# Kernel tuning notes

Measured on AMD Instinct MI355X. Metric: run time of the kernel, lower is better.

The kernel has to match this reference:

```python
import jax, jax.numpy as jnp
import numpy as np

N = 768        # nodes
F = 64         # invariant (0e) hidden channels
V = 16         # vector (1e) hidden channels
NB = 8         # bessel basis size
HR = 64        # radial MLP hidden
T = 2          # interactions
RO_S = 32      # invariant readout channels
RO_V = 16      # vector readout channels
RMAX = 10.0
AVG = float(N - 1)   # avg_num_neighbors (fully connected)
P = F + V + F + V + V  # tensor-product paths: s*Y0->0e, dot(v,Y1)->0e, s*Y1->1e, v*Y0->1e, cross(v,Y1)->1e


def _edges(n):
    # fully connected neighbor list (cut_off = 1e6, no pbc): all i != j
    s, r = np.meshgrid(np.arange(n), np.arange(n), indexing='ij')
    m = s != r
    return jnp.asarray(s[m]), jnp.asarray(r[m])


def _bessel(r):
    # bessel_basis(number=NB): sqrt(2/r_max) * sin(n*pi*r/r_max) / r
    n = jnp.arange(1, NB + 1, dtype=r.dtype)
    return jnp.sqrt(2.0 / RMAX) * jnp.sin(n * jnp.pi * r[:, None] / RMAX) / r[:, None]


def _envelope(r):
    # soft_envelope: 1.2 * sus(2*(1 - r/r_max)), sus(u) = exp(-1/u) for u>0 else 0
    u = 2.0 * (1.0 - r / RMAX)
    safe = jnp.where(u > 0, u, 1.0)
    return 1.2 * jnp.where(u > 0, jnp.exp(-1.0 / safe), 0.0)


def setup_inputs() -> dict:
    key = jax.random.key(0)
    ks = jax.random.split(key, 12)
    rn = lambda k, shp, fan: jax.random.normal(k, shp, jnp.float32) / np.sqrt(fan)
    return {
        'x': jax.random.normal(ks[0], (N, 3), jnp.float32),
        'embed': rn(ks[1], (1, F), 1),
        'w_node_s': rn(ks[2], (T, F, F), F),
        'w_node_v': rn(ks[3], (T, V, V), V),
        'w_rad1': rn(ks[4], (T, NB, HR), NB),
        'b_rad1': jnp.zeros((T, HR), jnp.float32),
        'w_rad2': rn(ks[5], (T, HR, P), HR),
        'w_mix_s': rn(ks[6], (T, F + V, F), F + V),
        'w_mix_v': rn(ks[7], (T, F + 2 * V, V), F + 2 * V),
        'w_gate': rn(ks[8], (T, F, V), F),
        'w_ro_s': rn(ks[9], (T, F, RO_S), F),
        'w_ro_v': rn(ks[10], (T, V, RO_V), V),
    }


def reference(x, embed, w_node_s, w_node_v, w_rad1, b_rad1, w_rad2,
              w_mix_s, w_mix_v, w_gate, w_ro_s, w_ro_v):
    n = x.shape[0]
    com = jnp.mean(x, axis=-2)                       # [3] centre of mass
    senders, receivers = _edges(n)
    vec = x[receivers] - x[senders]                  # [E,3] edge relative vectors
    r = jnp.linalg.norm(vec, axis=-1)                # [E]
    rhat = vec / r[:, None]                          # Y1 spherical harmonics (l=1)
    rb = _bessel(r)                                  # [E,NB]
    env = _envelope(r)                               # [E]

    h_s = jnp.broadcast_to(embed[0], (n, F))         # species embedding (all species 0)
    h_v = jnp.zeros((n, V, 3), x.dtype)
    out_s = jnp.zeros((n, RO_S), x.dtype)
    out_v = jnp.zeros((n, RO_V, 3), x.dtype)

    for t in range(T):
        # node-wise linear before gather
        hs = h_s @ w_node_s[t]                                    # [N,F]
        hv = jnp.einsum('nvc,vw->nwc', h_v, w_node_v[t])          # [N,V,3]
        es = hs[senders]                                          # [E,F]
        ev = hv[senders]                                          # [E,V,3]
        # per-edge tensor-product path weights from radial MLP, enveloped
        R = jax.nn.silu(rb @ w_rad1[t] + b_rad1[t]) @ w_rad2[t] * env[:, None]  # [E,P]
        r1, r2, r3, r4, r5 = (R[:, :F], R[:, F:F + V], R[:, F + V:2 * F + V],
                              R[:, 2 * F + V:2 * F + 2 * V], R[:, 2 * F + 2 * V:])
        # equivariant tensor products with Y0=1, Y1=rhat
        dot = jnp.einsum('evc,ec->ev', ev, rhat)                  # 1e x 1e -> 0e
        msg_s = jnp.concatenate([es * r1, dot * r2], axis=-1)     # [E,F+V]
        v1 = (es * r3)[:, :, None] * rhat[:, None, :]             # 0e x 1e -> 1e  [E,F,3]
        v2 = ev * r4[:, :, None]                                  # 1e x 0e -> 1e  [E,V,3]
        v3 = jnp.cross(ev, rhat[:, None, :]) * r5[:, :, None]     # 1e x 1e -> 1e  [E,V,3]
        msg_v = jnp.concatenate([v1, v2, v3], axis=1)             # [E,F+2V,3]
        # scatter-aggregate to receivers
        agg_s = jax.ops.segment_sum(msg_s, receivers, num_segments=n) / AVG
        agg_v = jax.ops.segment_sum(msg_v, receivers, num_segments=n) / AVG
        # mix + gated nonlinearity
        m_s = agg_s @ w_mix_s[t]                                  # [N,F]
        m_v = jnp.einsum('npc,pv->nvc', agg_v, w_mix_v[t])        # [N,V,3]
        h_s = jax.nn.silu(m_s)
        gate = jax.nn.sigmoid(m_s @ w_gate[t])                    # [N,V]
        h_v = gate[:, :, None] * m_v
        # readout (summed over interactions)
        out_s = out_s + h_s @ w_ro_s[t]
        out_v = out_v + jnp.einsum('nvc,vk->nkc', h_v, w_ro_v[t])

    return out_s, out_v + com
```

## Files before the change

### kernel.cpp

```cpp
#include <hip/hip_runtime.h>
#include <hip/hip_bf16.h>
#include <math.h>

#define Nn 768
#define Ff 64
#define Vv 16
#define NBb 8
#define HRr 64
#define Pp 176
#define TBL 1024
#define ROWC 176
#define RMAXF 10.0f
#define AVGF 767.0f
#define SCALE 102.4f

#define WS_COM   0
#define WS_ES0   16
#define WS_XP    128
#define WS_HSB   4096
#define WS_HVB   28672
#define WS_OS    53248
#define WS_OV    77824
#define WS_SLAB0 131072
#define WS_SLAB1 917504
#define WS_TBL   2097152

__device__ __forceinline__ unsigned short f2bf(float f) {
  unsigned b = __float_as_uint(f);
  return (unsigned short)((b + 0x7fffu + ((b >> 16) & 1u)) >> 16);
}
__device__ __forceinline__ float lp(unsigned u, float f) {
  float a = __uint_as_float(u << 16);
  float b = __uint_as_float(u & 0xffff0000u);
  return fmaf(f, b - a, a);
}
__device__ __forceinline__ float bl(unsigned u) { return __uint_as_float(u << 16); }
__device__ __forceinline__ float bh(unsigned u) { return __uint_as_float(u & 0xffff0000u); }

__global__ __launch_bounds__(256) void k_setup(const float* __restrict__ x,
                                               const float* __restrict__ embed,
                                               const float* __restrict__ wns,
                                               const float* __restrict__ w1,
                                               const float* __restrict__ b1,
                                               const float* __restrict__ w2,
                                               float* __restrict__ ws) {
  const int b = blockIdx.x, tid = threadIdx.x;
  if (b >= 256) {
    if (b == 256) {
      __shared__ float red[256][3];
      float a0 = 0, a1 = 0, a2 = 0;
      for (int n = tid; n < Nn; n += 256) {
        a0 += x[n * 3 + 0]; a1 += x[n * 3 + 1]; a2 += x[n * 3 + 2];
      }
      red[tid][0] = a0; red[tid][1] = a1; red[tid][2] = a2;
      __syncthreads();
      if (tid < 3) {
        float a = 0;
        for (int k = 0; k < 256; ++k) a += red[k][tid];
        ws[WS_COM + tid] = a * (1.0f / Nn);
      }
    } else if (b == 257) {
      for (int n = tid; n < Nn; n += 256) {
        ws[WS_XP + n * 4 + 0] = x[n * 3 + 0];
        ws[WS_XP + n * 4 + 1] = x[n * 3 + 1];
        ws[WS_XP + n * 4 + 2] = x[n * 3 + 2];
        ws[WS_XP + n * 4 + 3] = 0.0f;
      }
    } else {
      if (tid < 64) {
        float a = 0;
        for (int k = 0; k < 64; ++k) a = fmaf(embed[k], wns[k * 64 + tid], a);
        ws[WS_ES0 + tid] = a;
      }
    }
    return;
  }
  __shared__ float w2s[64][Pp];
  __shared__ float w1s[NBb][64];
  __shared__ float b1s[64];
  __shared__ float hid[9][65];
  const int t = b >> 7;
  const int r0 = (b & 127) * 8;
  const float* W2 = w2 + t * HRr * Pp;
  for (int k = tid; k < 64 * Pp; k += 256) w2s[k / Pp][k % Pp] = W2[k];
  for (int k = tid; k < NBb * 64; k += 256) w1s[k >> 6][k & 63] = w1[t * NBb * 64 + k];
  if (tid < 64) b1s[tid] = b1[t * 64 + tid];
  __syncthreads();
  {
    int rl4 = tid >> 6, h = tid & 63;
    const float c0 = 0.447213595f;
    const float pif = 3.14159265358979f;
    for (int pass = 0; pass < 3; ++pass) {
      int row_l = pass * 4 + rl4;
      if (row_l < 9) {
        int row = r0 + row_l;
        float r = row * (RMAXF / TBL);
        float acc = b1s[h];
        if (row == 0) {
          for (int n = 0; n < NBb; ++n) acc = fmaf(c0 * (n + 1) * (pif / RMAXF), w1s[n][h], acc);
        } else {
          float inv = 1.0f / r;
          for (int n = 0; n < NBb; ++n)
            acc = fmaf(c0 * sinf((n + 1) * pif * r / RMAXF) * inv, w1s[n][h], acc);
        }
        hid[row_l][h] = acc / (1.0f + expf(-acc));
      }
    }
  }
  __syncthreads();
  unsigned* T = (unsigned*)(ws + WS_TBL) + t * 1025 * ROWC;
  const int rl = tid & 7, colg = tid >> 3;
  const int rowa = r0 + rl;
  float ra = rowa * (RMAXF / TBL), rb = (rowa + 1) * (RMAXF / TBL);
  float ua = 2.0f * (1.0f - ra / RMAXF), ub = 2.0f * (1.0f - rb / RMAXF);
  float env_a = (ua > 0.0f) ? 1.2f * expf(-1.0f / ua) : 0.0f;
  float env_b = (ub > 0.0f) ? 1.2f * expf(-1.0f / ub) : 0.0f;
  float accA[6], accB[6];
  int pcol[6]; bool vc[6];
#pragma unroll
  for (int c = 0; c < 6; ++c) {
    int col = colg * 6 + c;
    bool valid = (col < 176);
    int p = 0;
    if (valid) {
      if (col < 64) p = col;
      else if (col < 128) p = 80 + (col - 64);
      else if (col < 144) p = 64 + (col - 128);
      else p = col;
    }
    pcol[c] = p; vc[c] = valid; accA[c] = 0.0f; accB[c] = 0.0f;
  }
  for (int h = 0; h < 64; ++h) {
    float ha = hid[rl][h], hb = hid[rl + 1][h];
#pragma unroll
    for (int c = 0; c < 6; ++c) {
      float w = w2s[h][pcol[c]];
      accA[c] = fmaf(ha, w, accA[c]);
      accB[c] = fmaf(hb, w, accB[c]);
    }
  }
#pragma unroll
  for (int c = 0; c < 6; ++c) {
    if (vc[c]) {
      int col = colg * 6 + c;
      float va = accA[c] * env_a;
      float vb = accB[c] * env_b;
      T[rowa * ROWC + col] = ((unsigned)f2bf(vb) << 16) | (unsigned)f2bf(va);
    }
  }
  if ((b & 127) == 127) {
    for (int k = tid; k < ROWC; k += 256) T[1024 * ROWC + k] = 0u;
  }
}

__global__ __launch_bounds__(256) void k_edge0(float* __restrict__ ws) {
  const int blk = blockIdx.x, i = blk >> 2, part = blk & 3;
  const int tid = threadIdx.x;
  const int w = tid >> 6, lane = tid & 63, sq = (lane >> 4) & 3, idx = lane & 15;
  __shared__ float4 GEO[192];
  __shared__ float wb[4][16][17];
  const float4* XP4 = (const float4*)(ws + WS_XP);
  const unsigned* T0 = (const unsigned*)(ws + WS_TBL);
  const float4 xi = XP4[i];
  if (tid < 192) {
    int j = part * 192 + tid;
    float4 xj = XP4[j];
    float dx = xi.x - xj.x, dy = xi.y - xj.y, dz = xi.z - xj.z;
    float r2 = dx * dx + dy * dy + dz * dz;
    float u, hx, hy, hz;
    if (j == i || r2 <= 0.0f) { u = 1024.0f; hx = hy = hz = 0.0f; }
    else {
      float rinv = rsqrtf(r2);
      hx = dx * rinv; hy = dy * rinv; hz = dz * rinv;
      u = fminf(r2 * rinv * SCALE, 1024.0f);
    }
    GEO[tid] = make_float4(hx, hy, hz, u);
  }
  __syncthreads();
  float s1[4] = {0, 0, 0, 0};
  float v1[4][3] = {};
  const int base = w * 48 + sq;
  float4 g = GEO[base];
  int i0 = (int)g.w;
  float fr = g.w - (float)i0;
  const uint4* rp = (const uint4*)(T0 + i0 * ROWC);
  uint4 t1 = rp[idx];
  uint4 t3 = rp[16 + idx];
  for (int q = 0; q < 12; ++q) {
    float4 gc = g; float frc = fr;
    uint4 t1c = t1, t3c = t3;
    if (q < 11) {
      g = GEO[base + (q + 1) * 4];
      i0 = (int)g.w;
      fr = g.w - (float)i0;
      const uint4* rpn = (const uint4*)(T0 + i0 * ROWC);
      t1 = rpn[idx];
      t3 = rpn[16 + idx];
    }
    s1[0] += lp(t1c.x, frc); s1[1] += lp(t1c.y, frc);
    s1[2] += lp(t1c.z, frc); s1[3] += lp(t1c.w, frc);
    float ax = lp(t3c.x, frc), ay = lp(t3c.y, frc), az = lp(t3c.z, frc), aw = lp(t3c.w, frc);
    v1[0][0] += ax * gc.x; v1[0][1] += ax * gc.y; v1[0][2] += ax * gc.z;
    v1[1][0] += ay * gc.x; v1[1][1] += ay * gc.y; v1[1][2] += ay * gc.z;
    v1[2][0] += az * gc.x; v1[2][1] += az * gc.y; v1[2][2] += az * gc.z;
    v1[3][0] += aw * gc.x; v1[3][1] += aw * gc.y; v1[3][2] += aw * gc.z;
  }
  float vals[16] = {s1[0], s1[1], s1[2], s1[3],
                    v1[0][0], v1[0][1], v1[0][2], v1[1][0], v1[1][1], v1[1][2],
                    v1[2][0], v1[2][1], v1[2][2], v1[3][0], v1[3][1], v1[3][2]};
#pragma unroll
  for (int k = 0; k < 16; ++k) {
    float v = vals[k];
    v += __shfl_xor(v, 16);
    v += __shfl_xor(v, 32);
    if (lane < 16) wb[w][lane][k] = v;
  }
  __syncthreads();
  {
    int l, s;
    if (tid < 64) { l = tid >> 2; s = tid & 3; }
    else { int p = tid - 64, f = p / 3, c = p - 3 * f; l = f >> 2; s = 4 + 3 * (f & 3) + c; }
    float a = wb[0][l][s] + wb[1][l][s] + wb[2][l][s] + wb[3][l][s];
    ws[WS_SLAB0 + (part * Nn + i) * 256 + tid] = a;
  }
}

__global__ __launch_bounds__(256) void k_post0(const float* __restrict__ wns,
                                               const float* __restrict__ wnv,
                                               const float* __restrict__ wmixs,
                                               const float* __restrict__ wmixv,
                                               const float* __restrict__ wgate,
                                               const float* __restrict__ wros,
                                               const float* __restrict__ wrov,
                                               float* __restrict__ ws) {
  const int i = blockIdx.x, tid = threadIdx.x;
  __shared__ float agg[256];
  __shared__ float ms[64], mvv[16][3], gate[16], hsn[64], hvns[16][4];
  __shared__ float hs1s[64], hv1s[16][4];
  const float inv = 1.0f / AVGF;
  const float* S = ws + WS_SLAB0 + i * 256;
  {
    float a = S[tid] + S[Nn * 256 + tid] + S[2 * Nn * 256 + tid] + S[3 * Nn * 256 + tid];
    float es0f = (tid < 64) ? ws[WS_ES0 + tid] : ws[WS_ES0 + (tid - 64) / 3];
    agg[tid] = a * inv * es0f;
  }
  __syncthreads();
  if (tid < 64) {
    const float* Wm = wmixs;
    float a = 0;
    for (int p = 0; p < 64; ++p) a = fmaf(agg[p], Wm[p * 64 + tid], a);
    ms[tid] = a;
  } else if (tid < 112) {
    int c = (tid - 64) >> 4, v = (tid - 64) & 15;
    const float* Wv = wmixv;
    float a = 0;
    for (int p = 0; p < 64; ++p) a = fmaf(agg[64 + p * 3 + c], Wv[p * 16 + v], a);
    mvv[v][c] = a;
  }
  __syncthreads();
  if (tid < 64) {
    float m = ms[tid];
    hsn[tid] = m / (1.0f + expf(-m));
  } else if (tid < 80) {
    int v = tid - 64;
    float a = 0;
    for (int f = 0; f < 64; ++f) a = fmaf(ms[f], wgate[f * 16 + v], a);
    gate[v] = 1.0f / (1.0f + expf(-a));
  }
  __syncthreads();
  if (tid < 64) {
    int v = tid >> 2, c = tid & 3;
    hvns[v][c] = (c < 3) ? gate[v] * mvv[v][c] : 0.0f;
  }
  __syncthreads();
  if (tid < 32) {
    float a = 0;
    for (int f = 0; f < 64; ++f) a = fmaf(hsn[f], wros[f * 32 + tid], a);
    ws[WS_OS + i * 32 + tid] = a;
  } else if (tid < 80) {
    int p = tid - 32, k = p / 3, c = p - 3 * k;
    float a = 0;
    for (int v = 0; v < 16; ++v) a = fmaf(hvns[v][c], wrov[v * 16 + k], a);
    ws[WS_OV + i * 48 + p] = a;
  } else if (tid < 144) {
    int f2 = tid - 80;
    const float* Wn = wns + 64 * 64;
    float a = 0;
    for (int f = 0; f < 64; ++f) a = fmaf(hsn[f], Wn[f * 64 + f2], a);
    hs1s[f2] = a;
  } else if (tid < 208) {
    int s = tid - 144, wv = s >> 2, c = s & 3;
    float a = 0;
    if (c < 3) {
      const float* Wn = wnv + 16 * 16;
      for (int v = 0; v < 16; ++v) a = fmaf(hvns[v][c], Wn[v * 16 + wv], a);
    }
    hv1s[wv][c] = a;
  }
  __syncthreads();
  if (tid < 16) {
    uint2* HSB = (uint2*)(ws + WS_HSB);
    unsigned u0 = (unsigned)f2bf(hs1s[4 * tid + 0]) | ((unsigned)f2bf(hs1s[4 * tid + 1]) << 16);
    unsigned u1 = (unsigned)f2bf(hs1s[4 * tid + 2]) | ((unsigned)f2bf(hs1s[4 * tid + 3]) << 16);
    HSB[i * 16 + tid] = make_uint2(u0, u1);
  } else if (tid < 32) {
    int v = tid - 16;
    uint2* HVB = (uint2*)(ws + WS_HVB);
    unsigned u0 = (unsigned)f2bf(hv1s[v][0]) | ((unsigned)f2bf(hv1s[v][1]) << 16);
    unsigned u1 = (unsigned)f2bf(hv1s[v][2]);
    HVB[i * 16 + v] = make_uint2(u0, u1);
  }
}

__global__ __launch_bounds__(256) void k_edge1(float* __restrict__ ws) {
  const int blk = blockIdx.x, i = blk >> 2, part = blk & 3;
  const int tid = threadIdx.x;
  const int w = tid >> 6, lane = tid & 63, sq = (lane >> 4) & 3, idx = lane & 15;
  __shared__ float4 GEO[192];
  __shared__ float wb[4][16][25];
  const float4* XP4 = (const float4*)(ws + WS_XP);
  const unsigned* T1 = (const unsigned*)(ws + WS_TBL) + 1025 * ROWC;
  const uint2* HSB = (const uint2*)(ws + WS_HSB);
  const uint2* HVB = (const uint2*)(ws + WS_HVB);
  const float4 xi = XP4[i];
  if (tid < 192) {
    int j = part * 192 + tid;
    float4 xj = XP4[j];
    float dx = xi.x - xj.x, dy = xi.y - xj.y, dz = xi.z - xj.z;
    float r2 = dx * dx + dy * dy + dz * dz;
    float u, hx, hy, hz;
    if (j == i || r2 <= 0.0f) { u = 1024.0f; hx = hy = hz = 0.0f; }
    else {
      float rinv = rsqrtf(r2);
      hx = dx * rinv; hy = dy * rinv; hz = dz * rinv;
      u = fminf(r2 * rinv * SCALE, 1024.0f);
    }
    GEO[tid] = make_float4(hx, hy, hz, u);
  }
  __syncthreads();
  float s1[4] = {0, 0, 0, 0};
  float v1[4][3] = {};
  float s2 = 0, v2x = 0, v2y = 0, v2z = 0, v3x = 0, v3y = 0, v3z = 0;
  const int jbase = part * 192;
  const int base = w * 48 + sq;
  float4 g = GEO[base];
  int i0 = (int)g.w;
  float fr = g.w - (float)i0;
  const unsigned* row = T1 + i0 * ROWC;
  uint4 t1 = ((const uint4*)row)[idx];
  uint4 t3 = ((const uint4*)row)[16 + idx];
  unsigned u2 = row[128 + idx];
  unsigned u4 = row[144 + idx];
  unsigned u5 = row[160 + idx];
  uint2 esb = HSB[(jbase + base) * 16 + idx];
  uint2 evb = HVB[(jbase + base) * 16 + idx];
  for (int q = 0; q < 12; ++q) {
    float4 gc = g; float frc = fr;
    uint4 t1c = t1, t3c = t3;
    unsigned u2c = u2, u4c = u4, u5c = u5;
    uint2 esc = esb, evc = evb;
    if (q < 11) {
      int jl = base + (q + 1) * 4;
      g = GEO[jl];
      i0 = (int)g.w;
      fr = g.w - (float)i0;
      const unsigned* rn = T1 + i0 * ROWC;
      t1 = ((const uint4*)rn)[idx];
      t3 = ((const uint4*)rn)[16 + idx];
      u2 = rn[128 + idx];
      u4 = rn[144 + idx];
      u5 = rn[160 + idx];
      esb = HSB[(jbase + jl) * 16 + idx];
      evb = HVB[(jbase + jl) * 16 + idx];
    }
    float esx = bl(esc.x), esy = bh(esc.x), esz = bl(esc.y), esw = bh(esc.y);
    float evx = bl(evc.x), evy = bh(evc.x), evz = bl(evc.y);
    s1[0] += esx * lp(t1c.x, frc); s1[1] += esy * lp(t1c.y, frc);
    s1[2] += esz * lp(t1c.z, frc); s1[3] += esw * lp(t1c.w, frc);
    float ax = esx * lp(t3c.x, frc), ay = esy * lp(t3c.y, frc);
    float az = esz * lp(t3c.z, frc), aw = esw * lp(t3c.w, frc);
    v1[0][0] += ax * gc.x; v1[0][1] += ax * gc.y; v1[0][2] += ax * gc.z;
    v1[1][0] += ay * gc.x; v1[1][1] += ay * gc.y; v1[1][2] += ay * gc.z;
    v1[2][0] += az * gc.x; v1[2][1] += az * gc.y; v1[2][2] += az * gc.z;
    v1[3][0] += aw * gc.x; v1[3][1] += aw * gc.y; v1[3][2] += aw * gc.z;
    float rr2 = lp(u2c, frc), rr4 = lp(u4c, frc), rr5 = lp(u5c, frc);
    float dt = evx * gc.x + evy * gc.y + evz * gc.z;
    s2 += dt * rr2;
    v2x += evx * rr4; v2y += evy * rr4; v2z += evz * rr4;
    v3x += (evy * gc.z - evz * gc.y) * rr5;
    v3y += (evz * gc.x - evx * gc.z) * rr5;
    v3z += (evx * gc.y - evy * gc.x) * rr5;
  }
  float vals[23] = {s1[0], s1[1], s1[2], s1[3],
                    v1[0][0], v1[0][1], v1[0][2], v1[1][0], v1[1][1], v1[1][2],
                    v1[2][0], v1[2][1], v1[2][2], v1[3][0], v1[3][1], v1[3][2],
                    s2, v2x, v2y, v2z, v3x, v3y, v3z};
#pragma unroll
  for (int k = 0; k < 23; ++k) {
    float v = vals[k];
    v += __shfl_xor(v, 16);
    v += __shfl_xor(v, 32);
    if (lane < 16) wb[w][lane][k] = v;
  }
  __syncthreads();
  for (int s = tid; s < 368; s += 256) {
    int l, sl;
    if (s < 64) { l = s >> 2; sl = s & 3; }
    else if (s < 80) { l = s - 64; sl = 16; }
    else if (s < 272) { int p = s - 80, f = p / 3, c = p - 3 * f; l = f >> 2; sl = 4 + 3 * (f & 3) + c; }
    else if (s < 320) { int p = s - 272, v = p / 3, c = p - 3 * v; l = v; sl = 17 + c; }
    else { int p = s - 320, v = p / 3, c = p - 3 * v; l = v; sl = 20 + c; }
    ws[WS_SLAB1 + (part * Nn + i) * 384 + s] =
        wb[0][l][sl] + wb[1][l][sl] + wb[2][l][sl] + wb[3][l][sl];
  }
}

__global__ __launch_bounds__(256) void k_post1(const float* __restrict__ wmixs,
                                               const float* __restrict__ wmixv,
                                               const float* __restrict__ wgate,
                                               const float* __restrict__ wros,
                                               const float* __restrict__ wrov,
                                               float* __restrict__ ws,
                                               float* __restrict__ out) {
  const int i = blockIdx.x, tid = threadIdx.x;
  __shared__ float agg[368];
  __shared__ float ms[64], mvv[16][3], gate[16], hsn[64], hvns[16][4];
  const float inv = 1.0f / AVGF;
  const float* S = ws + WS_SLAB1 + i * 384;
  for (int s = tid; s < 368; s += 256)
    agg[s] = (S[s] + S[Nn * 384 + s] + S[2 * Nn * 384 + s] + S[3 * Nn * 384 + s]) * inv;
  __syncthreads();
  if (tid < 64) {
    const float* Wm = wmixs + 80 * 64;
    float a = 0;
    for (int p = 0; p < 80; ++p) a = fmaf(agg[p], Wm[p * 64 + tid], a);
    ms[tid] = a;
  } else if (tid < 112) {
    int c = (tid - 64) >> 4, v = (tid - 64) & 15;
    const float* Wv = wmixv + 96 * 16;
    float a = 0;
    for (int p = 0; p < 96; ++p) {
      int ai = (p < 64) ? (80 + p * 3 + c) : (p < 80 ? (272 + (p - 64) * 3 + c)
                                                     : (320 + (p - 80) * 3 + c));
      a = fmaf(agg[ai], Wv[p * 16 + v], a);
    }
    mvv[v][c] = a;
  }
  __syncthreads();
  if (tid < 64) {
    float m = ms[tid];
    hsn[tid] = m / (1.0f + expf(-m));
  } else if (tid < 80) {
    int v = tid - 64;
    const float* Wg = wgate + 64 * 16;
    float a = 0;
    for (int f = 0; f < 64; ++f) a = fmaf(ms[f], Wg[f * 16 + v], a);
    gate[v] = 1.0f / (1.0f + expf(-a));
  }
  __syncthreads();
  if (tid < 64) {
    int v = tid >> 2, c = tid & 3;
    hvns[v][c] = (c < 3) ? gate[v] * mvv[v][c] : 0.0f;
  }
  __syncthreads();
  if (tid < 32) {
    const float* Wr = wros + 64 * 32;
    float a = ws[WS_OS + i * 32 + tid];
    for (int f = 0; f < 64; ++f) a = fmaf(hsn[f], Wr[f * 32 + tid], a);
    out[i * 32 + tid] = a;
  } else if (tid < 80) {
    int p = tid - 32, k = p / 3, c = p - 3 * k;
    const float* Wr = wrov + 16 * 16;
    float a = ws[WS_OV + i * 48 + p] + ws[WS_COM + c];
    for (int v = 0; v < 16; ++v) a = fmaf(hvns[v][c], Wr[v * 16 + k], a);
    out[Nn * 32 + i * 48 + p] = a;
  }
}

extern "C" void kernel_launch(void* const* d_in, const int* in_sizes, int n_in,
                              void* d_out, int out_size, void* d_ws, size_t ws_size,
                              hipStream_t stream) {
  const float* x     = (const float*)d_in[0];
  const float* embed = (const float*)d_in[1];
  const float* wns   = (const float*)d_in[2];
  const float* wnv   = (const float*)d_in[3];
  const float* w1    = (const float*)d_in[4];
  const float* b1    = (const float*)d_in[5];
  const float* w2    = (const float*)d_in[6];
  const float* wmixs = (const float*)d_in[7];
  const float* wmixv = (const float*)d_in[8];
  const float* wgate = (const float*)d_in[9];
  const float* wros  = (const float*)d_in[10];
  const float* wrov  = (const float*)d_in[11];
  float* ws = (float*)d_ws;
  float* out = (float*)d_out;

  hipLaunchKernelGGL(k_setup, dim3(259),    dim3(256), 0, stream, x, embed, wns, w1, b1, w2, ws);
  hipLaunchKernelGGL(k_edge0, dim3(Nn * 4), dim3(256), 0, stream, ws);
  hipLaunchKernelGGL(k_post0, dim3(Nn),     dim3(256), 0, stream,
                     wns, wnv, wmixs, wmixv, wgate, wros, wrov, ws);
  hipLaunchKernelGGL(k_edge1, dim3(Nn * 4), dim3(256), 0, stream, ws);
  hipLaunchKernelGGL(k_post1, dim3(Nn),     dim3(256), 0, stream,
                     wmixs, wmixv, wgate, wros, wrov, ws, out);
}
```

Before: 152.9 us.

## Fuse edge and post kernels into one 1024-thread block per node

Each interaction now runs a single kernel per receiver node with 1024 threads (16 waves), instead of four 256-thread edge blocks followed by a separate post kernel. All 768 senders are reduced inside one block through shared memory, which removes the global slab writes and reads and two kernel launches. The cost is fewer, larger blocks and more shared memory per block. Once the edge phase ends, most of the 1024 threads sit idle during the serial mixing and readout phase, which lowers effective occupancy.

```diff
diff --git a/kernel.cpp b/kernel.cpp
--- a/kernel.cpp
+++ b/kernel.cpp
@@ -21,8 +21,6 @@
 #define WS_HVB   28672
 #define WS_OS    53248
 #define WS_OV    77824
-#define WS_SLAB0 131072
-#define WS_SLAB1 917504
 #define WS_TBL   2097152
 
 __device__ __forceinline__ unsigned short f2bf(float f) {
@@ -153,17 +151,26 @@
   }
 }
 
-__global__ __launch_bounds__(256) void k_edge0(float* __restrict__ ws) {
-  const int blk = blockIdx.x, i = blk >> 2, part = blk & 3;
-  const int tid = threadIdx.x;
-  const int w = tid >> 6, lane = tid & 63, sq = (lane >> 4) & 3, idx = lane & 15;
-  __shared__ float4 GEO[192];
-  __shared__ float wb[4][16][17];
+__global__ __launch_bounds__(1024, 4) void k_fused0(const float* __restrict__ wns,
+                                                    const float* __restrict__ wnv,
+                                                    const float* __restrict__ wmixs,
+                                                    const float* __restrict__ wmixv,
+                                                    const float* __restrict__ wgate,
+                                                    const float* __restrict__ wros,
+                                                    const float* __restrict__ wrov,
+                                                    float* __restrict__ ws) {
+  const int i = blockIdx.x, tid = threadIdx.x;
+  const int w16 = tid >> 6, lane = tid & 63, sq = (lane >> 4) & 3, idx = lane & 15;
+  __shared__ float4 GEO[768];
+  __shared__ float wb[16][16][17];
+  __shared__ float agg[256];
+  __shared__ float ms[64], mvv[16][3], gate[16], hsn[64], hvns[16][4];
+  __shared__ float hs1s[64], hv1s[16][4];
   const float4* XP4 = (const float4*)(ws + WS_XP);
   const unsigned* T0 = (const unsigned*)(ws + WS_TBL);
   const float4 xi = XP4[i];
-  if (tid < 192) {
-    int j = part * 192 + tid;
+  if (tid < 768) {
+    int j = tid;
     float4 xj = XP4[j];
     float dx = xi.x - xj.x, dy = xi.y - xj.y, dz = xi.z - xj.z;
     float r2 = dx * dx + dy * dy + dz * dz;
@@ -179,7 +186,7 @@
   __syncthreads();
   float s1[4] = {0, 0, 0, 0};
   float v1[4][3] = {};
-  const int base = w * 48 + sq;
+  const int base = w16 * 48 + sq;
   float4 g = GEO[base];
   int i0 = (int)g.w;
   float fr = g.w - (float)i0;
@@ -213,48 +220,28 @@
     float v = vals[k];
     v += __shfl_xor(v, 16);
     v += __shfl_xor(v, 32);
-    if (lane < 16) wb[w][lane][k] = v;
-  }
-  __syncthreads();
-  {
-    int l, s;
-    if (tid < 64) { l = tid >> 2; s = tid & 3; }
-    else { int p = tid - 64, f = p / 3, c = p - 3 * f; l = f >> 2; s = 4 + 3 * (f & 3) + c; }
-    float a = wb[0][l][s] + wb[1][l][s] + wb[2][l][s] + wb[3][l][s];
-    ws[WS_SLAB0 + (part * Nn + i) * 256 + tid] = a;
-  }
-}
-
-__global__ __launch_bounds__(256) void k_post0(const float* __restrict__ wns,
-                                               const float* __restrict__ wnv,
-                                               const float* __restrict__ wmixs,
-                                               const float* __restrict__ wmixv,
-                                               const float* __restrict__ wgate,
-                                               const float* __restrict__ wros,
-                                               const float* __restrict__ wrov,
-                                               float* __restrict__ ws) {
-  const int i = blockIdx.x, tid = threadIdx.x;
-  __shared__ float agg[256];
-  __shared__ float ms[64], mvv[16][3], gate[16], hsn[64], hvns[16][4];
-  __shared__ float hs1s[64], hv1s[16][4];
-  const float inv = 1.0f / AVGF;
-  const float* S = ws + WS_SLAB0 + i * 256;
-  {
-    float a = S[tid] + S[Nn * 256 + tid] + S[2 * Nn * 256 + tid] + S[3 * Nn * 256 + tid];
+    if (lane < 16) wb[w16][lane][k] = v;
+  }
+  __syncthreads();
+  if (tid < 256) {
+    int l, sl;
+    if (tid < 64) { l = tid >> 2; sl = tid & 3; }
+    else { int p = tid - 64, f = p / 3, c = p - 3 * f; l = f >> 2; sl = 4 + 3 * (f & 3) + c; }
+    float a = 0;
+#pragma unroll
+    for (int wv = 0; wv < 16; ++wv) a += wb[wv][l][sl];
     float es0f = (tid < 64) ? ws[WS_ES0 + tid] : ws[WS_ES0 + (tid - 64) / 3];
-    agg[tid] = a * inv * es0f;
-  }
-  __syncthreads();
-  if (tid < 64) {
-    const float* Wm = wmixs;
-    float a = 0;
-    for (int p = 0; p < 64; ++p) a = fmaf(agg[p], Wm[p * 64 + tid], a);
+    agg[tid] = a * (1.0f / AVGF) * es0f;
+  }
+  __syncthreads();
+  if (tid < 64) {
+    float a = 0;
+    for (int p = 0; p < 64; ++p) a = fmaf(agg[p], wmixs[p * 64 + tid], a);
     ms[tid] = a;
   } else if (tid < 112) {
     int c = (tid - 64) >> 4, v = (tid - 64) & 15;
-    const float* Wv = wmixv;
-    float a = 0;
-    for (int p = 0; p < 64; ++p) a = fmaf(agg[64 + p * 3 + c], Wv[p * 16 + v], a);
+    float a = 0;
+    for (int p = 0; p < 64; ++p) a = fmaf(agg[64 + p * 3 + c], wmixv[p * 16 + v], a);
     mvv[v][c] = a;
   }
   __syncthreads();
@@ -312,19 +299,26 @@
   }
 }
 
-__global__ __launch_bounds__(256) void k_edge1(float* __restrict__ ws) {
-  const int blk = blockIdx.x, i = blk >> 2, part = blk & 3;
-  const int tid = threadIdx.x;
-  const int w = tid >> 6, lane = tid & 63, sq = (lane >> 4) & 3, idx = lane & 15;
-  __shared__ float4 GEO[192];
-  __shared__ float wb[4][16][25];
+__global__ __launch_bounds__(1024, 4) void k_fused1(const float* __restrict__ wmixs,
+                                                    const float* __restrict__ wmixv,
+                                                    const float* __restrict__ wgate,
+                                                    const float* __restrict__ wros,
+                                                    const float* __restrict__ wrov,
+                                                    float* __restrict__ ws,
+                                                    float* __restrict__ out) {
+  const int i = blockIdx.x, tid = threadIdx.x;
+  const int w16 = tid >> 6, lane = tid & 63, sq = (lane >> 4) & 3, idx = lane & 15;
+  __shared__ float4 GEO[768];
+  __shared__ float wb[16][16][25];
+  __shared__ float agg[368];
+  __shared__ float ms[64], mvv[16][3], gate[16], hsn[64], hvns[16][4];
   const float4* XP4 = (const float4*)(ws + WS_XP);
   const unsigned* T1 = (const unsigned*)(ws + WS_TBL) + 1025 * ROWC;
   const uint2* HSB = (const uint2*)(ws + WS_HSB);
   const uint2* HVB = (const uint2*)(ws + WS_HVB);
   const float4 xi = XP4[i];
-  if (tid < 192) {
-    int j = part * 192 + tid;
+  if (tid < 768) {
+    int j = tid;
     float4 xj = XP4[j];
     float dx = xi.x - xj.x, dy = xi.y - xj.y, dz = xi.z - xj.z;
     float r2 = dx * dx + dy * dy + dz * dz;
@@ -341,8 +335,7 @@
   float s1[4] = {0, 0, 0, 0};
   float v1[4][3] = {};
   float s2 = 0, v2x = 0, v2y = 0, v2z = 0, v3x = 0, v3y = 0, v3z = 0;
-  const int jbase = part * 192;
-  const int base = w * 48 + sq;
+  const int base = w16 * 48 + sq;
   float4 g = GEO[base];
   int i0 = (int)g.w;
   float fr = g.w - (float)i0;
@@ -352,8 +345,8 @@
   unsigned u2 = row[128 + idx];
   unsigned u4 = row[144 + idx];
   unsigned u5 = row[160 + idx];
-  uint2 esb = HSB[(jbase + base) * 16 + idx];
-  uint2 evb = HVB[(jbase + base) * 16 + idx];
+  uint2 esb = HSB[base * 16 + idx];
+  uint2 evb = HVB[base * 16 + idx];
   for (int q = 0; q < 12; ++q) {
     float4 gc = g; float frc = fr;
     uint4 t1c = t1, t3c = t3;
@@ -370,8 +363,8 @@
       u2 = rn[128 + idx];
       u4 = rn[144 + idx];
       u5 = rn[160 + idx];
-      esb = HSB[(jbase + jl) * 16 + idx];
-      evb = HVB[(jbase + jl) * 16 + idx];
+      esb = HSB[jl * 16 + idx];
+      evb = HVB[jl * 16 + idx];
     }
     float esx = bl(esc.x), esy = bh(esc.x), esz = bl(esc.y), esw = bh(esc.y);
     float evx = bl(evc.x), evy = bh(evc.x), evz = bl(evc.y);
@@ -400,35 +393,21 @@
     float v = vals[k];
     v += __shfl_xor(v, 16);
     v += __shfl_xor(v, 32);
-    if (lane < 16) wb[w][lane][k] = v;
-  }
-  __syncthreads();
-  for (int s = tid; s < 368; s += 256) {
+    if (lane < 16) wb[w16][lane][k] = v;
+  }
+  __syncthreads();
+  if (tid < 368) {
     int l, sl;
-    if (s < 64) { l = s >> 2; sl = s & 3; }
-    else if (s < 80) { l = s - 64; sl = 16; }
-    else if (s < 272) { int p = s - 80, f = p / 3, c = p - 3 * f; l = f >> 2; sl = 4 + 3 * (f & 3) + c; }
-    else if (s < 320) { int p = s - 272, v = p / 3, c = p - 3 * v; l = v; sl = 17 + c; }
-    else { int p = s - 320, v = p / 3, c = p - 3 * v; l = v; sl = 20 + c; }
-    ws[WS_SLAB1 + (part * Nn + i) * 384 + s] =
-        wb[0][l][sl] + wb[1][l][sl] + wb[2][l][sl] + wb[3][l][sl];
-  }
-}
-
-__global__ __launch_bounds__(256) void k_post1(const float* __restrict__ wmixs,
-                                               const float* __restrict__ wmixv,
-                                               const float* __restrict__ wgate,
-                                               const float* __restrict__ wros,
-                                               const float* __restrict__ wrov,
-                                               float* __restrict__ ws,
-                                               float* __restrict__ out) {
-  const int i = blockIdx.x, tid = threadIdx.x;
-  __shared__ float agg[368];
-  __shared__ float ms[64], mvv[16][3], gate[16], hsn[64], hvns[16][4];
-  const float inv = 1.0f / AVGF;
-  const float* S = ws + WS_SLAB1 + i * 384;
-  for (int s = tid; s < 368; s += 256)
-    agg[s] = (S[s] + S[Nn * 384 + s] + S[2 * Nn * 384 + s] + S[3 * Nn * 384 + s]) * inv;
+    if (tid < 64) { l = tid >> 2; sl = tid & 3; }
+    else if (tid < 80) { l = tid - 64; sl = 16; }
+    else if (tid < 272) { int p = tid - 80, f = p / 3, c = p - 3 * f; l = f >> 2; sl = 4 + 3 * (f & 3) + c; }
+    else if (tid < 320) { int p = tid - 272, v = p / 3, c = p - 3 * v; l = v; sl = 17 + c; }
+    else { int p = tid - 320, v = p / 3, c = p - 3 * v; l = v; sl = 20 + c; }
+    float a = 0;
+#pragma unroll
+    for (int wv = 0; wv < 16; ++wv) a += wb[wv][l][sl];
+    agg[tid] = a * (1.0f / AVGF);
+  }
   __syncthreads();
   if (tid < 64) {
     const float* Wm = wmixs + 80 * 64;
@@ -495,11 +474,9 @@
   float* ws = (float*)d_ws;
   float* out = (float*)d_out;
 
-  hipLaunchKernelGGL(k_setup, dim3(259),    dim3(256), 0, stream, x, embed, wns, w1, b1, w2, ws);
-  hipLaunchKernelGGL(k_edge0, dim3(Nn * 4), dim3(256), 0, stream, ws);
-  hipLaunchKernelGGL(k_post0, dim3(Nn),     dim3(256), 0, stream,
+  hipLaunchKernelGGL(k_setup,  dim3(259), dim3(256),  0, stream, x, embed, wns, w1, b1, w2, ws);
+  hipLaunchKernelGGL(k_fused0, dim3(Nn),  dim3(1024), 0, stream,
                      wns, wnv, wmixs, wmixv, wgate, wros, wrov, ws);
-  hipLaunchKernelGGL(k_edge1, dim3(Nn * 4), dim3(256), 0, stream, ws);
-  hipLaunchKernelGGL(k_post1, dim3(Nn),     dim3(256), 0, stream,
+  hipLaunchKernelGGL(k_fused1, dim3(Nn),  dim3(1024), 0, stream,
                      wmixs, wmixv, wgate, wros, wrov, ws, out);
 }
```

Result: slower. 190.7 us (+24.7%).
